# Optimization experiments

Measured on AMD Instinct MI355X. Metric: run time of the kernel, lower is better.

Reference implementation:

```python
import jax, jax.numpy as jnp
import numpy as np

N_VARS = 16
BATCH = 16
SEQ = 512
P = N_VARS * (N_VARS - 1)  # ordered pairs i != j


def setup_inputs() -> dict:
    key = jax.random.key(0)
    ks = jax.random.split(key, 12)
    n = N_VARS

    def w(k, shape, fan_in):
        return jax.random.normal(k, shape, dtype=jnp.float32) / np.sqrt(fan_in)

    z = lambda *s: jnp.zeros(s, jnp.float32)
    return {
        'data': jax.random.normal(ks[0], (BATCH, SEQ, n), dtype=jnp.float32),
        # structure learner: n*n -> 256 -> 128 -> n*n (dropout skipped / eval mode)
        'Ws1': w(ks[1], (n * n, 256), n * n), 'bs1': z(256),
        'Ws2': w(ks[2], (256, 128), 256), 'bs2': z(128),
        'Ws3': w(ks[3], (128, n * n), 128), 'bs3': z(n * n),
        # per-variable causal mechanisms (stacked): (n-1) -> 128 -> 64 -> 1
        'Wm1': w(ks[4], (n, n - 1, 128), n - 1), 'bm1': z(n, 128),
        'Wm2': w(ks[5], (n, 128, 64), 128), 'bm2': z(n, 64),
        'Wm3': w(ks[6], (n, 64), 64), 'bm3': z(n),
        # per-pair independence tests (stacked): 2 -> 32 -> 1, sigmoid
        'Wt1': w(ks[7], (P, 2, 32), 2), 'bt1': z(P, 32),
        'Wt2': w(ks[8], (P, 32), 32), 'bt2': z(P),
    }


def reference(data, Ws1, bs1, Ws2, bs2, Ws3, bs3,
              Wm1, bm1, Wm2, bm2, Wm3, bm3,
              Wt1, bt1, Wt2, bt2):
    B, S, n = data.shape
    N = B * S
    flat = data.reshape(N, n)  # [N, n] all samples

    # ---- correlations of batch-averaged series (vectorized corrcoef) ----
    avg = data.mean(axis=0)                    # [S, n]
    xc = avg - avg.mean(axis=0, keepdims=True)
    cov = xc.T @ xc                            # [n, n]
    std = jnp.sqrt(jnp.clip(jnp.diag(cov), 0.0))
    denom = std[:, None] * std[None, :]
    corr = jnp.abs(jnp.where(denom > 0, cov / jnp.where(denom > 0, denom, 1.0), 0.0))
    corr = corr * (1.0 - jnp.eye(n, dtype=corr.dtype))  # zero diagonal (i != j only)

    # ---- structure learner MLP -> sigmoid -> strict upper-tri DAG mask ----
    h = jax.nn.relu(corr.reshape(1, -1) @ Ws1 + bs1)
    h = jax.nn.relu(h @ Ws2 + bs2)
    adj = jax.nn.sigmoid(h @ Ws3 + bs3).reshape(n, n)
    adj = jnp.triu(adj, 1)

    # ---- causal mechanisms: gather-parents -> per-var MLP -> scatter ----
    idx = np.stack([[j for j in range(n) if j != v] for v in range(n)])  # [n, n-1]
    pmask = adj > 0.5
    parent_mask = pmask[idx, np.arange(n)[:, None]].astype(flat.dtype)   # [n, n-1]
    inp = flat[:, idx] * parent_mask[None]                               # [N, n, n-1]
    h1 = jax.nn.relu(jnp.einsum('nvp,vph->nvh', inp, Wm1) + bm1)         # [N, n, 128]
    h2 = jax.nn.relu(jnp.einsum('nvh,vhk->nvk', h1, Wm2) + bm2)          # [N, n, 64]
    mech = jnp.einsum('nvk,vk->nv', h2, Wm3) + bm3                       # [N, n]
    has_parents = parent_mask.sum(axis=1) > 0                            # [n]
    predictions = jnp.where(has_parents[None, :], mech, flat).reshape(B, S, n)

    # ---- batched per-pair independence tests ----
    pairs = np.array([(i, j) for i in range(n) for j in range(n) if i != j])
    pi, pj = pairs[:, 0], pairs[:, 1]
    X = jnp.stack([flat[:, pi], flat[:, pj]], axis=-1)                   # [N, P, 2]
    ht = jax.nn.relu(jnp.einsum('npc,pch->nph', X, Wt1) + bt1)           # [N, P, 32]
    s = jax.nn.sigmoid(jnp.einsum('nph,ph->np', ht, Wt2) + bt2).mean(axis=0)  # [P]
    scores = jnp.zeros((n, n), flat.dtype).at[pi, pj].set(s)

    return adj, predictions, scores
```

## Files before the change

### kernel.cpp

```cpp
#include <hip/hip_runtime.h>
#include <hip/hip_bf16.h>


typedef __attribute__((ext_vector_type(8))) short bf16x8;
typedef __attribute__((ext_vector_type(4))) short bf16x4;
typedef __attribute__((ext_vector_type(4))) float f32x4;

#define DEV __device__ __forceinline__
DEV short f2bf(float f){ __hip_bfloat16 h = __float2bfloat16(f); short s; __builtin_memcpy(&s,&h,2); return s; }

struct GraphSm {
    float avT[16 * 532];
    float part[512];
    float corr[256];
    float h1[256];
    float h2[128];
    float adj[256];
};
struct MechSm {
    short W2T[64 * 136];
    short H1[8][16 * 136];
    float W1[16 * 128];
    float B1[128];
    float B2[64];
    float W3[64];
};
struct PairSm {
    float w0[2][32], w1[2][32], bb[2][32], w2[2][32];
    float red[2][512];
    float b2s[2];
};
union SmU { GraphSm g; MechSm m; PairSm p; };

__global__ void __launch_bounds__(512, 2) k_fused(
    const float* __restrict__ data,
    const float* __restrict__ Ws1, const float* __restrict__ bs1,
    const float* __restrict__ Ws2, const float* __restrict__ bs2,
    const float* __restrict__ Ws3, const float* __restrict__ bs3,
    const float* __restrict__ Wm1, const float* __restrict__ bm1,
    const float* __restrict__ Wm2, const float* __restrict__ bm2,
    const float* __restrict__ Wm3, const float* __restrict__ bm3,
    const float* __restrict__ Wt1, const float* __restrict__ bt1,
    const float* __restrict__ Wt2, const float* __restrict__ bt2,
    float* __restrict__ out)
{
    __shared__ __align__(16) SmU sm;
    int tid = threadIdx.x, bid = blockIdx.x;

    if (bid >= 128) {
        int pb = bid - 128;
        int p0 = pb*2, p1 = p0 + 1;
        int i0 = p0 / 15, jr0 = p0 % 15;
        int j0 = jr0 + (jr0 >= i0 ? 1 : 0);
        int i1 = p1 / 15, jr1 = p1 % 15;
        int j1 = jr1 + (jr1 >= i1 ? 1 : 0);
        if (tid < 64) {
            int pp = tid >> 5, h = tid & 31;
            int p = pb*2 + pp;
            sm.p.w0[pp][h] = Wt1[p*64 + h];
            sm.p.w1[pp][h] = Wt1[p*64 + 32 + h];
            sm.p.bb[pp][h] = bt1[p*32 + h];
            sm.p.w2[pp][h] = Wt2[p*32 + h];
        }
        if (tid < 2) sm.p.b2s[tid] = bt2[pb*2 + tid];
        __syncthreads();
        float b2s0 = sm.p.b2s[0], b2s1 = sm.p.b2s[1];
        float acc0 = 0.f, acc1 = 0.f;
        float nxa0, nxb0, nxa1, nxb1;
        {
            int s = ((bid & 15) * 512) + tid;
            nxa0 = data[s*16 + i0]; nxb0 = data[s*16 + j0];
            nxa1 = data[s*16 + i1]; nxb1 = data[s*16 + j1];
        }
        for (int it = 0; it < 16; ++it) {
            float xa0 = nxa0, xb0 = nxb0, xa1 = nxa1, xb1 = nxb1;
            if (it < 15) {
                int s = (((it + 1 + bid) & 15) * 512) + tid;
                nxa0 = data[s*16 + i0]; nxb0 = data[s*16 + j0];
                nxa1 = data[s*16 + i1]; nxb1 = data[s*16 + j1];
            }
            float za0=0.f, zb0=0.f, za1=0.f, zb1=0.f;
            #pragma unroll
            for (int h = 0; h < 32; h += 2) {
                float t00 = fmaf(xa0, sm.p.w0[0][h],   fmaf(xb0, sm.p.w1[0][h],   sm.p.bb[0][h]));
                za0 = fmaf(fmaxf(t00, 0.f), sm.p.w2[0][h],   za0);
                float t01 = fmaf(xa0, sm.p.w0[0][h+1], fmaf(xb0, sm.p.w1[0][h+1], sm.p.bb[0][h+1]));
                zb0 = fmaf(fmaxf(t01, 0.f), sm.p.w2[0][h+1], zb0);
                float t10 = fmaf(xa1, sm.p.w0[1][h],   fmaf(xb1, sm.p.w1[1][h],   sm.p.bb[1][h]));
                za1 = fmaf(fmaxf(t10, 0.f), sm.p.w2[1][h],   za1);
                float t11 = fmaf(xa1, sm.p.w0[1][h+1], fmaf(xb1, sm.p.w1[1][h+1], sm.p.bb[1][h+1]));
                zb1 = fmaf(fmaxf(t11, 0.f), sm.p.w2[1][h+1], zb1);
            }
            float z0 = b2s0 + za0 + zb0;
            float z1 = b2s1 + za1 + zb1;
            acc0 += __builtin_amdgcn_rcpf(1.f + __expf(-z0));
            acc1 += __builtin_amdgcn_rcpf(1.f + __expf(-z1));
        }
        sm.p.red[0][tid] = acc0;
        sm.p.red[1][tid] = acc1;
        __syncthreads();
        for (int off = 256; off > 0; off >>= 1) {
            if (tid < off) {
                sm.p.red[0][tid] += sm.p.red[0][tid + off];
                sm.p.red[1][tid] += sm.p.red[1][tid + off];
            }
            __syncthreads();
        }
        if (tid == 0) {
            out[256 + 131072 + i0*16 + j0] = sm.p.red[0][0] * (1.f/8192.f);
            out[256 + 131072 + i1*16 + j1] = sm.p.red[1][0] * (1.f/8192.f);
        }
        return;
    }

    int v = bid >> 3, chunk = bid & 7;
    int gs0 = chunk * 1024;

    float pf_wm1[4];
    {
        #pragma unroll
        for (int r = 0; r < 4; ++r) {
            int e = tid + 512*r;
            int k = e >> 7, h = e & 127;
            pf_wm1[r] = 0.f;
            if (k != v) {
                int p = k - (k > v ? 1 : 0);
                pf_wm1[r] = Wm1[v*1920 + p*128 + h];
            }
        }
    }
    float4 pf_wm2[4];
    {
        const float* wp = Wm2 + v*8192 + tid*16;
        #pragma unroll
        for (int m4 = 0; m4 < 4; ++m4) pf_wm2[m4] = *(const float4*)&wp[m4*4];
    }
    float b1r  = bm1[v*128 + (tid & 127)];
    float b2r_ = bm2[v*64  + (tid & 63)];
    float w3r  = Wm3[v*64  + (tid & 63)];
    float bm3v = bm3[v];
    float bs1r = bs1[tid & 255];
    float bs2r = bs2[tid & 127];
    float bs3r = bs3[tid & 255];

    {
        int vb = (tid & 3) * 4;
        int sgr = ((tid >> 2) + bid*4) & 127;
        for (int k = 0; k < 4; ++k) {
            int s = sgr + k*128;
            float ax=0.f, ay=0.f, az=0.f, aw=0.f;
            #pragma unroll
            for (int b = 0; b < 16; ++b) {
                float4 d4 = *(const float4*)&data[b*8192 + s*16 + vb];
                ax += d4.x; ay += d4.y; az += d4.z; aw += d4.w;
            }
            sm.g.avT[(vb+0)*532 + s] = ax * 0.0625f;
            sm.g.avT[(vb+1)*532 + s] = ay * 0.0625f;
            sm.g.avT[(vb+2)*532 + s] = az * 0.0625f;
            sm.g.avT[(vb+3)*532 + s] = aw * 0.0625f;
        }
    }
    __syncthreads();
    if (tid < 128) {
        int vv = tid >> 3, sgm = tid & 7;
        const float* rp = &sm.g.avT[vv*532 + sgm*64];
        float a0=0.f, a1=0.f, a2=0.f, a3=0.f;
        for (int s = 0; s < 64; s += 4) {
            float4 fa = *(const float4*)&rp[s];
            a0 += fa.x; a1 += fa.y; a2 += fa.z; a3 += fa.w;
        }
        sm.g.h2[tid] = (a0+a1)+(a2+a3);
    }
    __syncthreads();
    int ci, cj; float mci, mcj;
    {
        int t = tid & 255, hh = tid >> 8;
        ci = t >> 4; cj = t & 15;
        mci = 0.f; mcj = 0.f;
        #pragma unroll
        for (int q = 0; q < 8; ++q) { mci += sm.g.h2[ci*8 + q]; mcj += sm.g.h2[cj*8 + q]; }
        mci *= (1.f/512.f); mcj *= (1.f/512.f);
        const float* pi_ = &sm.g.avT[ci*532 + hh*256];
        const float* pj_ = &sm.g.avT[cj*532 + hh*256];
        float a0=0.f, a1=0.f, a2=0.f, a3=0.f;
        #pragma unroll 8
        for (int s = 0; s < 256; s += 4) {
            float4 fa = *(const float4*)&pi_[s];
            float4 fb = *(const float4*)&pj_[s];
            a0 = fmaf(fa.x, fb.x, a0); a1 = fmaf(fa.y, fb.y, a1);
            a2 = fmaf(fa.z, fb.z, a2); a3 = fmaf(fa.w, fb.w, a3);
        }
        sm.g.part[tid] = (a0+a1)+(a2+a3);
    }
    __syncthreads();
    if (tid < 256) {
        float cij = sm.g.part[tid] + sm.g.part[256 + tid] - 512.f*mci*mcj;
        float cii = sm.g.part[ci*17] + sm.g.part[256 + ci*17] - 512.f*mci*mci;
        float cjj = sm.g.part[cj*17] + sm.g.part[256 + cj*17] - 512.f*mcj*mcj;
        float den = sqrtf(fmaxf(cii, 0.f)) * sqrtf(fmaxf(cjj, 0.f));
        sm.g.corr[tid] = (den > 0.f && ci != cj) ? fabsf(cij/den) : 0.f;
    }
    __syncthreads();

    float* red2 = sm.g.avT;

    {
        int o4 = tid & 63, ks = tid >> 6;
        int o4e = (o4 + bid*4) & 63;
        const float* W1p = Ws1 + ks*32*256 + o4e*4;
        const float* cp  = sm.g.corr + ks*32;
        float ax=0.f, ay=0.f, az=0.f, aw=0.f;
        float bx=0.f, by=0.f, bz=0.f, bw=0.f;
        #pragma unroll 8
        for (int i = 0; i < 32; i += 2) {
            float4 w0 = *(const float4*)&W1p[(i  )*256];
            float4 w1 = *(const float4*)&W1p[(i+1)*256];
            float c0 = cp[i], c1 = cp[i+1];
            ax=fmaf(c0,w0.x,ax); ay=fmaf(c0,w0.y,ay); az=fmaf(c0,w0.z,az); aw=fmaf(c0,w0.w,aw);
            bx=fmaf(c1,w1.x,bx); by=fmaf(c1,w1.y,by); bz=fmaf(c1,w1.z,bz); bw=fmaf(c1,w1.w,bw);
        }
        float4 r4; r4.x=ax+bx; r4.y=ay+by; r4.z=az+bz; r4.w=aw+bw;
        *(float4*)&red2[ks*256 + o4e*4] = r4;
    }
    __syncthreads();
    if (tid < 256) {
        float s = bs1r;
        #pragma unroll
        for (int k2 = 0; k2 < 8; ++k2) s += red2[k2*256 + tid];
        sm.g.h1[tid] = fmaxf(s, 0.f);
    }
    __syncthreads();
    {
        int o4 = tid & 31, ks = tid >> 5;
        int o4e = (o4 + bid*2) & 31;
        const float* W2p = Ws2 + ks*16*128 + o4e*4;
        const float* cp  = sm.g.h1 + ks*16;
        float ax=0.f, ay=0.f, az=0.f, aw=0.f;
        float bx=0.f, by=0.f, bz=0.f, bw=0.f;
        #pragma unroll
        for (int i = 0; i < 16; i += 2) {
            float4 w0 = *(const float4*)&W2p[(i  )*128];
            float4 w1 = *(const float4*)&W2p[(i+1)*128];
            float c0 = cp[i], c1 = cp[i+1];
            ax=fmaf(c0,w0.x,ax); ay=fmaf(c0,w0.y,ay); az=fmaf(c0,w0.z,az); aw=fmaf(c0,w0.w,aw);
            bx=fmaf(c1,w1.x,bx); by=fmaf(c1,w1.y,by); bz=fmaf(c1,w1.z,bz); bw=fmaf(c1,w1.w,bw);
        }
        float4 r4; r4.x=ax+bx; r4.y=ay+by; r4.z=az+bz; r4.w=aw+bw;
        *(float4*)&red2[ks*128 + o4e*4] = r4;
    }
    __syncthreads();
    if (tid < 128) {
        float s = bs2r;
        #pragma unroll
        for (int k2 = 0; k2 < 16; ++k2) s += red2[k2*128 + tid];
        sm.g.h2[tid] = fmaxf(s, 0.f);
    }
    __syncthreads();
    {
        int o4 = tid & 63, ks = tid >> 6;
        int o4e = (o4 + bid*4) & 63;
        const float* W3p = Ws3 + ks*16*256 + o4e*4;
        const float* cp  = sm.g.h2 + ks*16;
        float ax=0.f, ay=0.f, az=0.f, aw=0.f;
        float bx=0.f, by=0.f, bz=0.f, bw=0.f;
        #pragma unroll
        for (int i = 0; i < 16; i += 2) {
            float4 w0 = *(const float4*)&W3p[(i  )*256];
            float4 w1 = *(const float4*)&W3p[(i+1)*256];
            float c0 = cp[i], c1 = cp[i+1];
            ax=fmaf(c0,w0.x,ax); ay=fmaf(c0,w0.y,ay); az=fmaf(c0,w0.z,az); aw=fmaf(c0,w0.w,aw);
            bx=fmaf(c1,w1.x,bx); by=fmaf(c1,w1.y,by); bz=fmaf(c1,w1.z,bz); bw=fmaf(c1,w1.w,bw);
        }
        float4 r4; r4.x=ax+bx; r4.y=ay+by; r4.z=az+bz; r4.w=aw+bw;
        *(float4*)&red2[ks*256 + o4e*4] = r4;
    }
    __syncthreads();
    if (tid < 256) {
        float z = bs3r;
        #pragma unroll
        for (int k2 = 0; k2 < 8; ++k2) z += red2[k2*256 + tid];
        float a = 1.f / (1.f + expf(-z));
        int r = tid >> 4, cc = tid & 15;
        float adjv = (r < cc) ? a : 0.f;
        sm.g.adj[tid] = adjv;
        if (bid == 0) out[tid] = adjv;
    }
    if (bid == 0 && tid >= 256 && tid < 272)
        out[256 + 131072 + (tid-256)*17] = 0.f;
    __syncthreads();

    #pragma unroll
    for (int r = 0; r < 4; ++r) {
        int e = tid + 512*r;
        int k = e >> 7;
        float val = 0.f;
        if (k != v && sm.g.adj[k*16 + v] > 0.5f) val = pf_wm1[r];
        sm.m.W1[e] = val;
    }
    float hp = 0.f;
    #pragma unroll
    for (int k = 0; k < 16; ++k)
        if (k != v && sm.g.adj[k*16 + v] > 0.5f) hp = 1.f;
    #pragma unroll
    for (int m4 = 0; m4 < 4; ++m4) {
        float4 w4 = pf_wm2[m4];
        int e0 = tid*16 + m4*4;
        int h = e0 >> 6;
        int jj0 = e0 & 63;
        sm.m.W2T[(jj0+0)*136 + h] = f2bf(w4.x);
        sm.m.W2T[(jj0+1)*136 + h] = f2bf(w4.y);
        sm.m.W2T[(jj0+2)*136 + h] = f2bf(w4.z);
        sm.m.W2T[(jj0+3)*136 + h] = f2bf(w4.w);
    }
    if (tid < 128) sm.m.B1[tid] = b1r;
    else if (tid < 192) sm.m.B2[tid - 128] = b2r_;
    else if (tid < 256) sm.m.W3[tid - 192] = w3r;
    __syncthreads();

    int lane = tid & 63, wid = tid >> 6;
    int c = lane & 15, q = lane >> 4;

    bf16x8 a1f[8];
    #pragma unroll
    for (int ht = 0; ht < 8; ++ht) {
        #pragma unroll
        for (int jj = 0; jj < 8; ++jj) {
            int k = q*8 + jj;
            float w = (k < 16) ? sm.m.W1[k*128 + ht*16 + c] : 0.f;
            a1f[ht][jj] = f2bf(w);
        }
    }
    bf16x8 b2r[16];
    #pragma unroll
    for (int jt = 0; jt < 4; ++jt)
        #pragma unroll
        for (int ks = 0; ks < 4; ++ks)
            b2r[jt*4 + ks] = *(const bf16x8*)&sm.m.W2T[(jt*16 + c)*136 + ks*32 + q*8];
    float w3c[4], b2c[4];
    #pragma unroll
    for (int jt = 0; jt < 4; ++jt) { w3c[jt] = sm.m.W3[jt*16 + c]; b2c[jt] = sm.m.B2[jt*16 + c]; }

    short* h1buf = sm.m.H1[wid];
    bool act = (q < 2);

    float4 u0c, u1c;
    {
        int st0 = wid*8;
        if (act) {
            const float* xp = &data[(gs0 + st0*16 + c)*16 + q*8];
            u0c = *(const float4*)xp;
            u1c = *(const float4*)(xp + 4);
        }
    }

    for (int stl = 0; stl < 8; ++stl) {
        int st = wid*8 + stl;
        float4 u0 = u0c, u1 = u1c;
        if (stl < 7 && act) {
            const float* xp = &data[(gs0 + (st+1)*16 + c)*16 + q*8];
            u0c = *(const float4*)xp;
            u1c = *(const float4*)(xp + 4);
        }
        bf16x8 xb;
        #pragma unroll
        for (int i2 = 0; i2 < 8; ++i2) xb[i2] = 0;
        if (act) {
            xb[0] = f2bf(u0.x); xb[1] = f2bf(u0.y);
            xb[2] = f2bf(u0.z); xb[3] = f2bf(u0.w);
            xb[4] = f2bf(u1.x); xb[5] = f2bf(u1.y);
            xb[6] = f2bf(u1.z); xb[7] = f2bf(u1.w);
        }
        f32x4 c1[8];
        #pragma unroll
        for (int ht = 0; ht < 8; ++ht) c1[ht] = *(const f32x4*)&sm.m.B1[ht*16 + q*4];
        #pragma unroll
        for (int ht = 0; ht < 8; ++ht)
            c1[ht] = __builtin_amdgcn_mfma_f32_16x16x32_bf16(a1f[ht], xb, c1[ht], 0, 0, 0);
        #pragma unroll
        for (int ht = 0; ht < 8; ++ht) {
            bf16x4 pk;
            #pragma unroll
            for (int r = 0; r < 4; ++r) pk[r] = f2bf(fmaxf(c1[ht][r], 0.f));
            *(bf16x4*)&h1buf[c*136 + ht*16 + q*4] = pk;
        }
        f32x4 c2[4];
        #pragma unroll
        for (int jt = 0; jt < 4; ++jt) {
            float bi = b2c[jt];
            c2[jt] = (f32x4){bi, bi, bi, bi};
        }
        #pragma unroll
        for (int ks = 0; ks < 4; ++ks) {
            bf16x8 a2 = *(const bf16x8*)&h1buf[c*136 + ks*32 + q*8];
            #pragma unroll
            for (int jt = 0; jt < 4; ++jt)
                c2[jt] = __builtin_amdgcn_mfma_f32_16x16x32_bf16(a2, b2r[jt*4 + ks], c2[jt], 0, 0, 0);
        }
        float part[4];
        #pragma unroll
        for (int r = 0; r < 4; ++r) part[r] = 0.f;
        #pragma unroll
        for (int jt = 0; jt < 4; ++jt)
            #pragma unroll
            for (int r = 0; r < 4; ++r)
                part[r] = fmaf(fmaxf(c2[jt][r], 0.f), w3c[jt], part[r]);
        #pragma unroll
        for (int off = 1; off < 16; off <<= 1)
            #pragma unroll
            for (int r = 0; r < 4; ++r)
                part[r] += __shfl_xor(part[r], off, 16);
        if (c == 0) {
            #pragma unroll
            for (int r = 0; r < 4; ++r) {
                int s_loc = st*16 + q*4 + r;
                float mech = part[r] + bm3v;
                float xv = data[(gs0 + s_loc)*16 + v];
                out[256 + (gs0 + s_loc)*16 + v] = (hp != 0.f) ? mech : xv;
            }
        }
    }
}

extern "C" void kernel_launch(void* const* d_in, const int* in_sizes, int n_in,
                              void* d_out, int out_size, void* d_ws, size_t ws_size,
                              hipStream_t stream)
{
    const float* data = (const float*)d_in[0];
    const float* Ws1  = (const float*)d_in[1];
    const float* bs1  = (const float*)d_in[2];
    const float* Ws2  = (const float*)d_in[3];
    const float* bs2  = (const float*)d_in[4];
    const float* Ws3  = (const float*)d_in[5];
    const float* bs3  = (const float*)d_in[6];
    const float* Wm1  = (const float*)d_in[7];
    const float* bm1  = (const float*)d_in[8];
    const float* Wm2  = (const float*)d_in[9];
    const float* bm2  = (const float*)d_in[10];
    const float* Wm3  = (const float*)d_in[11];
    const float* bm3  = (const float*)d_in[12];
    const float* Wt1  = (const float*)d_in[13];
    const float* bt1  = (const float*)d_in[14];
    const float* Wt2  = (const float*)d_in[15];
    const float* bt2  = (const float*)d_in[16];
    float* out = (float*)d_out;
    (void)d_ws; (void)ws_size; (void)in_sizes; (void)n_in; (void)out_size;

    hipLaunchKernelGGL(k_fused, dim3(248), dim3(512), 0, stream,
                       data, Ws1, bs1, Ws2, bs2, Ws3, bs3,
                       Wm1, bm1, Wm2, bm2, Wm3, bm3,
                       Wt1, bt1, Wt2, bt2, out);
}
```

Baseline: 126.3 us.

## Compute graph structure once via cross-block flags instead of per-block redundancy

Result: slower. 158.8 us (+25.7%).

```diff
diff --git a/kernel.cpp b/kernel.cpp
--- a/kernel.cpp
+++ b/kernel.cpp
@@ -9,28 +9,38 @@
 #define DEV __device__ __forceinline__
 DEV short f2bf(float f){ __hip_bfloat16 h = __float2bfloat16(f); short s; __builtin_memcpy(&s,&h,2); return s; }
 
+#define WS_P1(b)   ((b)*272)
+#define WS_PM      8960
+#define WS_HP      9200
+#define WS_DUMMY   9400
+#define WS_FLAG    9600
+#define FLAG_MAGIC 0x1357F00D
+
 struct GraphSm {
-    float avT[16 * 532];
-    float part[512];
+    float sum1[256];
+    float m[16];
     float corr[256];
+    float red2[2048];
     float h1[256];
     float h2[128];
     float adj[256];
+    float pm[240];
 };
+struct ProdSm { float av[16*17]; };
 struct MechSm {
-    short W2T[64 * 136];
-    short H1[8][16 * 136];
-    float W1[16 * 128];
+    short W2T[64*136];
+    short H1[8][16*136];
+    float W1[16*128];
     float B1[128];
     float B2[64];
     float W3[64];
 };
 struct PairSm {
     float w0[2][32], w1[2][32], bb[2][32], w2[2][32];
-    float red[2][512];
+    float red0[8], red1[8];
     float b2s[2];
 };
-union SmU { GraphSm g; MechSm m; PairSm p; };
+union SmU { GraphSm g; ProdSm pr; MechSm m; PairSm p; };
 
 __global__ void __launch_bounds__(512, 2) k_fused(
     const float* __restrict__ data,
@@ -42,17 +52,19 @@
     const float* __restrict__ Wm3, const float* __restrict__ bm3,
     const float* __restrict__ Wt1, const float* __restrict__ bt1,
     const float* __restrict__ Wt2, const float* __restrict__ bt2,
-    float* __restrict__ out)
+    float* __restrict__ wsf, float* __restrict__ out)
 {
     __shared__ __align__(16) SmU sm;
+    __shared__ float pmhp[16];
     int tid = threadIdx.x, bid = blockIdx.x;
-
-    if (bid >= 128) {
-        int pb = bid - 128;
-        int p0 = pb*2, p1 = p0 + 1;
+    int* flags = (int*)(wsf + WS_FLAG);
+
+    if (bid >= 129) {
+        int pb = bid - 129;
+        int p0 = pb*2, p1p = p0 + 1;
         int i0 = p0 / 15, jr0 = p0 % 15;
         int j0 = jr0 + (jr0 >= i0 ? 1 : 0);
-        int i1 = p1 / 15, jr1 = p1 % 15;
+        int i1 = p1p / 15, jr1 = p1p % 15;
         int j1 = jr1 + (jr1 >= i1 ? 1 : 0);
         if (tid < 64) {
             int pp = tid >> 5, h = tid & 31;
@@ -66,18 +78,22 @@
         __syncthreads();
         float b2s0 = sm.p.b2s[0], b2s1 = sm.p.b2s[1];
         float acc0 = 0.f, acc1 = 0.f;
-        float nxa0, nxb0, nxa1, nxb1;
+        float a0A, b0A, a1A, b1A, a0B, b0B, a1B, b1B;
         {
-            int s = ((bid & 15) * 512) + tid;
-            nxa0 = data[s*16 + i0]; nxb0 = data[s*16 + j0];
-            nxa1 = data[s*16 + i1]; nxb1 = data[s*16 + j1];
+            int s0 = tid;
+            a0A = data[s0*16 + i0]; b0A = data[s0*16 + j0];
+            a1A = data[s0*16 + i1]; b1A = data[s0*16 + j1];
+            int s1 = 512 + tid;
+            a0B = data[s1*16 + i0]; b0B = data[s1*16 + j0];
+            a1B = data[s1*16 + i1]; b1B = data[s1*16 + j1];
         }
         for (int it = 0; it < 16; ++it) {
-            float xa0 = nxa0, xb0 = nxb0, xa1 = nxa1, xb1 = nxb1;
-            if (it < 15) {
-                int s = (((it + 1 + bid) & 15) * 512) + tid;
-                nxa0 = data[s*16 + i0]; nxb0 = data[s*16 + j0];
-                nxa1 = data[s*16 + i1]; nxb1 = data[s*16 + j1];
+            float xa0 = a0A, xb0 = b0A, xa1 = a1A, xb1 = b1A;
+            a0A = a0B; b0A = b0B; a1A = a1B; b1A = b1B;
+            if (it < 14) {
+                int s = (it + 2)*512 + tid;
+                a0B = data[s*16 + i0]; b0B = data[s*16 + j0];
+                a1B = data[s*16 + i1]; b1B = data[s*16 + j1];
             }
             float za0=0.f, zb0=0.f, za1=0.f, zb1=0.f;
             #pragma unroll
@@ -96,37 +112,211 @@
             acc0 += __builtin_amdgcn_rcpf(1.f + __expf(-z0));
             acc1 += __builtin_amdgcn_rcpf(1.f + __expf(-z1));
         }
-        sm.p.red[0][tid] = acc0;
-        sm.p.red[1][tid] = acc1;
-        __syncthreads();
-        for (int off = 256; off > 0; off >>= 1) {
-            if (tid < off) {
-                sm.p.red[0][tid] += sm.p.red[0][tid + off];
-                sm.p.red[1][tid] += sm.p.red[1][tid + off];
+        #pragma unroll
+        for (int off = 32; off > 0; off >>= 1) {
+            acc0 += __shfl_xor(acc0, off);
+            acc1 += __shfl_xor(acc1, off);
+        }
+        int lane = tid & 63, wid = tid >> 6;
+        if (lane == 0) { sm.p.red0[wid] = acc0; sm.p.red1[wid] = acc1; }
+        __syncthreads();
+        if (tid == 0) {
+            float s0 = 0.f, s1 = 0.f;
+            #pragma unroll
+            for (int w = 0; w < 8; ++w) { s0 += sm.p.red0[w]; s1 += sm.p.red1[w]; }
+            out[256 + 131072 + i0*16 + j0] = s0 * (1.f/8192.f);
+            out[256 + 131072 + i1*16 + j1] = s1 * (1.f/8192.f);
+        }
+        return;
+    }
+
+    if (bid == 0) {
+        float bs1r = bs1[tid & 255];
+        float bs2r = bs2[tid & 127];
+        float bs3r = bs3[tid & 255];
+        if (tid < 32) {
+            while (__hip_atomic_load(&flags[tid], __ATOMIC_ACQUIRE,
+                                     __HIP_MEMORY_SCOPE_AGENT) != FLAG_MAGIC)
+                __builtin_amdgcn_s_sleep(2);
+        }
+        __syncthreads();
+        __threadfence();
+        if (tid < 256) {
+            float p1 = 0.f;
+            #pragma unroll 8
+            for (int b = 0; b < 32; ++b) p1 += wsf[WS_P1(b) + tid];
+            sm.g.sum1[tid] = p1;
+        }
+        if (tid < 16) {
+            float ms = 0.f;
+            #pragma unroll 8
+            for (int b = 0; b < 32; ++b) ms += wsf[WS_P1(b) + 256 + tid];
+            sm.g.m[tid] = ms * (1.f/512.f);
+        }
+        __syncthreads();
+        if (tid < 256) {
+            int ci = tid >> 4, cj = tid & 15;
+            float mci = sm.g.m[ci], mcj = sm.g.m[cj];
+            float cij = sm.g.sum1[tid]   - 512.f*mci*mcj;
+            float cii = sm.g.sum1[ci*17] - 512.f*mci*mci;
+            float cjj = sm.g.sum1[cj*17] - 512.f*mcj*mcj;
+            float den = sqrtf(fmaxf(cii, 0.f)) * sqrtf(fmaxf(cjj, 0.f));
+            sm.g.corr[tid] = (den > 0.f && ci != cj) ? fabsf(cij/den) : 0.f;
+        }
+        __syncthreads();
+        {
+            int o4 = tid & 63, ks = tid >> 6;
+            const float* W1p = Ws1 + ks*32*256 + o4*4;
+            const float* cp  = sm.g.corr + ks*32;
+            float ax=0.f, ay=0.f, az=0.f, aw=0.f;
+            float bx=0.f, by=0.f, bz=0.f, bw=0.f;
+            #pragma unroll 8
+            for (int i = 0; i < 32; i += 2) {
+                float4 w0 = *(const float4*)&W1p[(i  )*256];
+                float4 w1 = *(const float4*)&W1p[(i+1)*256];
+                float c0 = cp[i], c1 = cp[i+1];
+                ax=fmaf(c0,w0.x,ax); ay=fmaf(c0,w0.y,ay); az=fmaf(c0,w0.z,az); aw=fmaf(c0,w0.w,aw);
+                bx=fmaf(c1,w1.x,bx); by=fmaf(c1,w1.y,by); bz=fmaf(c1,w1.z,bz); bw=fmaf(c1,w1.w,bw);
             }
-            __syncthreads();
-        }
+            float4 r4; r4.x=ax+bx; r4.y=ay+by; r4.z=az+bz; r4.w=aw+bw;
+            *(float4*)&sm.g.red2[ks*256 + o4*4] = r4;
+        }
+        __syncthreads();
+        if (tid < 256) {
+            float s = bs1r;
+            #pragma unroll
+            for (int k2 = 0; k2 < 8; ++k2) s += sm.g.red2[k2*256 + tid];
+            sm.g.h1[tid] = fmaxf(s, 0.f);
+        }
+        __syncthreads();
+        {
+            int o4 = tid & 31, ks = tid >> 5;
+            const float* W2p = Ws2 + ks*16*128 + o4*4;
+            const float* cp  = sm.g.h1 + ks*16;
+            float ax=0.f, ay=0.f, az=0.f, aw=0.f;
+            float bx=0.f, by=0.f, bz=0.f, bw=0.f;
+            #pragma unroll
+            for (int i = 0; i < 16; i += 2) {
+                float4 w0 = *(const float4*)&W2p[(i  )*128];
+                float4 w1 = *(const float4*)&W2p[(i+1)*128];
+                float c0 = cp[i], c1 = cp[i+1];
+                ax=fmaf(c0,w0.x,ax); ay=fmaf(c0,w0.y,ay); az=fmaf(c0,w0.z,az); aw=fmaf(c0,w0.w,aw);
+                bx=fmaf(c1,w1.x,bx); by=fmaf(c1,w1.y,by); bz=fmaf(c1,w1.z,bz); bw=fmaf(c1,w1.w,bw);
+            }
+            float4 r4; r4.x=ax+bx; r4.y=ay+by; r4.z=az+bz; r4.w=aw+bw;
+            *(float4*)&sm.g.red2[ks*128 + o4*4] = r4;
+        }
+        __syncthreads();
+        if (tid < 128) {
+            float s = bs2r;
+            #pragma unroll
+            for (int k2 = 0; k2 < 16; ++k2) s += sm.g.red2[k2*128 + tid];
+            sm.g.h2[tid] = fmaxf(s, 0.f);
+        }
+        __syncthreads();
+        {
+            int o4 = tid & 63, ks = tid >> 6;
+            const float* W3p = Ws3 + ks*16*256 + o4*4;
+            const float* cp  = sm.g.h2 + ks*16;
+            float ax=0.f, ay=0.f, az=0.f, aw=0.f;
+            float bx=0.f, by=0.f, bz=0.f, bw=0.f;
+            #pragma unroll
+            for (int i = 0; i < 16; i += 2) {
+                float4 w0 = *(const float4*)&W3p[(i  )*256];
+                float4 w1 = *(const float4*)&W3p[(i+1)*256];
+                float c0 = cp[i], c1 = cp[i+1];
+                ax=fmaf(c0,w0.x,ax); ay=fmaf(c0,w0.y,ay); az=fmaf(c0,w0.z,az); aw=fmaf(c0,w0.w,aw);
+                bx=fmaf(c1,w1.x,bx); by=fmaf(c1,w1.y,by); bz=fmaf(c1,w1.z,bz); bw=fmaf(c1,w1.w,bw);
+            }
+            float4 r4; r4.x=ax+bx; r4.y=ay+by; r4.z=az+bz; r4.w=aw+bw;
+            *(float4*)&sm.g.red2[ks*256 + o4*4] = r4;
+        }
+        __syncthreads();
+        if (tid < 256) {
+            float z = bs3r;
+            #pragma unroll
+            for (int k2 = 0; k2 < 8; ++k2) z += sm.g.red2[k2*256 + tid];
+            float a = 1.f / (1.f + expf(-z));
+            int r = tid >> 4, cc = tid & 15;
+            float adjv = (r < cc) ? a : 0.f;
+            sm.g.adj[tid] = adjv;
+            out[tid] = adjv;
+        }
+        if (tid >= 256 && tid < 272)
+            out[256 + 131072 + (tid-256)*17] = 0.f;
+        __syncthreads();
+        if (tid < 240) {
+            int vv = tid / 15, p = tid % 15;
+            int jj = p + (p >= vv ? 1 : 0);
+            float pmv = (sm.g.adj[jj*16 + vv] > 0.5f) ? 1.f : 0.f;
+            wsf[WS_PM + tid] = pmv;
+            sm.g.pm[tid] = pmv;
+        }
+        __syncthreads();
+        if (tid < 16) {
+            float s = 0.f;
+            #pragma unroll
+            for (int p = 0; p < 15; ++p) s += sm.g.pm[tid*15 + p];
+            wsf[WS_HP + tid] = (s > 0.f) ? 1.f : 0.f;
+        }
+        __syncthreads();
         if (tid == 0) {
-            out[256 + 131072 + i0*16 + j0] = sm.p.red[0][0] * (1.f/8192.f);
-            out[256 + 131072 + i1*16 + j1] = sm.p.red[1][0] * (1.f/8192.f);
+            __threadfence();
+            __hip_atomic_store(&flags[32], FLAG_MAGIC,
+                               __ATOMIC_RELEASE, __HIP_MEMORY_SCOPE_AGENT);
         }
         return;
     }
 
-    int v = bid >> 3, chunk = bid & 7;
+    int v = (bid - 1) >> 3, chunk = (bid - 1) & 7;
     int gs0 = chunk * 1024;
 
+    if (bid <= 32) {
+        int b = bid - 1;
+        if (tid < 256) {
+            int sl = tid >> 4, vv = tid & 15;
+            int s = b*16 + sl;
+            float acc = 0.f;
+            #pragma unroll
+            for (int bt = 0; bt < 16; ++bt) acc += data[bt*8192 + s*16 + vv];
+            sm.pr.av[sl*17 + vv] = acc * (1.f/16.f);
+        }
+        __syncthreads();
+        if (tid < 256) {
+            int i2 = tid >> 4, j2 = tid & 15;
+            float p1 = 0.f;
+            #pragma unroll
+            for (int r = 0; r < 16; ++r) p1 += sm.pr.av[r*17 + i2] * sm.pr.av[r*17 + j2];
+            wsf[WS_P1(b) + tid] = p1;
+        }
+        if (tid < 16) {
+            float ms = 0.f;
+            #pragma unroll
+            for (int r = 0; r < 16; ++r) ms += sm.pr.av[r*17 + tid];
+            wsf[WS_P1(b) + 256 + tid] = ms;
+        }
+        __syncthreads();
+        if (tid == 0) {
+            __threadfence();
+            __hip_atomic_store(&flags[b], FLAG_MAGIC,
+                               __ATOMIC_RELEASE, __HIP_MEMORY_SCOPE_AGENT);
+        }
+        unsigned xr = 0;
+        { uint4 u = ((const uint4*)Ws1)[b*512 + tid]; xr ^= u.x^u.y^u.z^u.w; }
+        if (tid < 256) { uint4 u = ((const uint4*)Ws2)[b*256 + tid];       xr ^= u.x^u.y^u.z^u.w; }
+        else           { uint4 u = ((const uint4*)Ws3)[b*256 + tid - 256]; xr ^= u.x^u.y^u.z^u.w; }
+        if (xr == 0x9E3779B9u) wsf[WS_DUMMY] = 0.f;
+    }
+
     float pf_wm1[4];
-    {
-        #pragma unroll
-        for (int r = 0; r < 4; ++r) {
-            int e = tid + 512*r;
-            int k = e >> 7, h = e & 127;
-            pf_wm1[r] = 0.f;
-            if (k != v) {
-                int p = k - (k > v ? 1 : 0);
-                pf_wm1[r] = Wm1[v*1920 + p*128 + h];
-            }
+    #pragma unroll
+    for (int r = 0; r < 4; ++r) {
+        int e = tid + 512*r;
+        int k = e >> 7, h = e & 127;
+        pf_wm1[r] = 0.f;
+        if (k != v) {
+            int p = k - (k > v ? 1 : 0);
+            pf_wm1[r] = Wm1[v*1920 + p*128 + h];
         }
     }
     float4 pf_wm2[4];
@@ -136,171 +326,10 @@
         for (int m4 = 0; m4 < 4; ++m4) pf_wm2[m4] = *(const float4*)&wp[m4*4];
     }
     float b1r  = bm1[v*128 + (tid & 127)];
-    float b2r_ = bm2[v*64  + (tid & 63)];
+    float b2rv = bm2[v*64  + (tid & 63)];
     float w3r  = Wm3[v*64  + (tid & 63)];
     float bm3v = bm3[v];
-    float bs1r = bs1[tid & 255];
-    float bs2r = bs2[tid & 127];
-    float bs3r = bs3[tid & 255];
-
-    {
-        int vb = (tid & 3) * 4;
-        int sgr = ((tid >> 2) + bid*4) & 127;
-        for (int k = 0; k < 4; ++k) {
-            int s = sgr + k*128;
-            float ax=0.f, ay=0.f, az=0.f, aw=0.f;
-            #pragma unroll
-            for (int b = 0; b < 16; ++b) {
-                float4 d4 = *(const float4*)&data[b*8192 + s*16 + vb];
-                ax += d4.x; ay += d4.y; az += d4.z; aw += d4.w;
-            }
-            sm.g.avT[(vb+0)*532 + s] = ax * 0.0625f;
-            sm.g.avT[(vb+1)*532 + s] = ay * 0.0625f;
-            sm.g.avT[(vb+2)*532 + s] = az * 0.0625f;
-            sm.g.avT[(vb+3)*532 + s] = aw * 0.0625f;
-        }
-    }
-    __syncthreads();
-    if (tid < 128) {
-        int vv = tid >> 3, sgm = tid & 7;
-        const float* rp = &sm.g.avT[vv*532 + sgm*64];
-        float a0=0.f, a1=0.f, a2=0.f, a3=0.f;
-        for (int s = 0; s < 64; s += 4) {
-            float4 fa = *(const float4*)&rp[s];
-            a0 += fa.x; a1 += fa.y; a2 += fa.z; a3 += fa.w;
-        }
-        sm.g.h2[tid] = (a0+a1)+(a2+a3);
-    }
-    __syncthreads();
-    int ci, cj; float mci, mcj;
-    {
-        int t = tid & 255, hh = tid >> 8;
-        ci = t >> 4; cj = t & 15;
-        mci = 0.f; mcj = 0.f;
-        #pragma unroll
-        for (int q = 0; q < 8; ++q) { mci += sm.g.h2[ci*8 + q]; mcj += sm.g.h2[cj*8 + q]; }
-        mci *= (1.f/512.f); mcj *= (1.f/512.f);
-        const float* pi_ = &sm.g.avT[ci*532 + hh*256];
-        const float* pj_ = &sm.g.avT[cj*532 + hh*256];
-        float a0=0.f, a1=0.f, a2=0.f, a3=0.f;
-        #pragma unroll 8
-        for (int s = 0; s < 256; s += 4) {
-            float4 fa = *(const float4*)&pi_[s];
-            float4 fb = *(const float4*)&pj_[s];
-            a0 = fmaf(fa.x, fb.x, a0); a1 = fmaf(fa.y, fb.y, a1);
-            a2 = fmaf(fa.z, fb.z, a2); a3 = fmaf(fa.w, fb.w, a3);
-        }
-        sm.g.part[tid] = (a0+a1)+(a2+a3);
-    }
-    __syncthreads();
-    if (tid < 256) {
-        float cij = sm.g.part[tid] + sm.g.part[256 + tid] - 512.f*mci*mcj;
-        float cii = sm.g.part[ci*17] + sm.g.part[256 + ci*17] - 512.f*mci*mci;
-        float cjj = sm.g.part[cj*17] + sm.g.part[256 + cj*17] - 512.f*mcj*mcj;
-        float den = sqrtf(fmaxf(cii, 0.f)) * sqrtf(fmaxf(cjj, 0.f));
-        sm.g.corr[tid] = (den > 0.f && ci != cj) ? fabsf(cij/den) : 0.f;
-    }
-    __syncthreads();
-
-    float* red2 = sm.g.avT;
-
-    {
-        int o4 = tid & 63, ks = tid >> 6;
-        int o4e = (o4 + bid*4) & 63;
-        const float* W1p = Ws1 + ks*32*256 + o4e*4;
-        const float* cp  = sm.g.corr + ks*32;
-        float ax=0.f, ay=0.f, az=0.f, aw=0.f;
-        float bx=0.f, by=0.f, bz=0.f, bw=0.f;
-        #pragma unroll 8
-        for (int i = 0; i < 32; i += 2) {
-            float4 w0 = *(const float4*)&W1p[(i  )*256];
-            float4 w1 = *(const float4*)&W1p[(i+1)*256];
-            float c0 = cp[i], c1 = cp[i+1];
-            ax=fmaf(c0,w0.x,ax); ay=fmaf(c0,w0.y,ay); az=fmaf(c0,w0.z,az); aw=fmaf(c0,w0.w,aw);
-            bx=fmaf(c1,w1.x,bx); by=fmaf(c1,w1.y,by); bz=fmaf(c1,w1.z,bz); bw=fmaf(c1,w1.w,bw);
-        }
-        float4 r4; r4.x=ax+bx; r4.y=ay+by; r4.z=az+bz; r4.w=aw+bw;
-        *(float4*)&red2[ks*256 + o4e*4] = r4;
-    }
-    __syncthreads();
-    if (tid < 256) {
-        float s = bs1r;
-        #pragma unroll
-        for (int k2 = 0; k2 < 8; ++k2) s += red2[k2*256 + tid];
-        sm.g.h1[tid] = fmaxf(s, 0.f);
-    }
-    __syncthreads();
-    {
-        int o4 = tid & 31, ks = tid >> 5;
-        int o4e = (o4 + bid*2) & 31;
-        const float* W2p = Ws2 + ks*16*128 + o4e*4;
-        const float* cp  = sm.g.h1 + ks*16;
-        float ax=0.f, ay=0.f, az=0.f, aw=0.f;
-        float bx=0.f, by=0.f, bz=0.f, bw=0.f;
-        #pragma unroll
-        for (int i = 0; i < 16; i += 2) {
-            float4 w0 = *(const float4*)&W2p[(i  )*128];
-            float4 w1 = *(const float4*)&W2p[(i+1)*128];
-            float c0 = cp[i], c1 = cp[i+1];
-            ax=fmaf(c0,w0.x,ax); ay=fmaf(c0,w0.y,ay); az=fmaf(c0,w0.z,az); aw=fmaf(c0,w0.w,aw);
-            bx=fmaf(c1,w1.x,bx); by=fmaf(c1,w1.y,by); bz=fmaf(c1,w1.z,bz); bw=fmaf(c1,w1.w,bw);
-        }
-        float4 r4; r4.x=ax+bx; r4.y=ay+by; r4.z=az+bz; r4.w=aw+bw;
-        *(float4*)&red2[ks*128 + o4e*4] = r4;
-    }
-    __syncthreads();
-    if (tid < 128) {
-        float s = bs2r;
-        #pragma unroll
-        for (int k2 = 0; k2 < 16; ++k2) s += red2[k2*128 + tid];
-        sm.g.h2[tid] = fmaxf(s, 0.f);
-    }
-    __syncthreads();
-    {
-        int o4 = tid & 63, ks = tid >> 6;
-        int o4e = (o4 + bid*4) & 63;
-        const float* W3p = Ws3 + ks*16*256 + o4e*4;
-        const float* cp  = sm.g.h2 + ks*16;
-        float ax=0.f, ay=0.f, az=0.f, aw=0.f;
-        float bx=0.f, by=0.f, bz=0.f, bw=0.f;
-        #pragma unroll
-        for (int i = 0; i < 16; i += 2) {
-            float4 w0 = *(const float4*)&W3p[(i  )*256];
-            float4 w1 = *(const float4*)&W3p[(i+1)*256];
-            float c0 = cp[i], c1 = cp[i+1];
-            ax=fmaf(c0,w0.x,ax); ay=fmaf(c0,w0.y,ay); az=fmaf(c0,w0.z,az); aw=fmaf(c0,w0.w,aw);
-            bx=fmaf(c1,w1.x,bx); by=fmaf(c1,w1.y,by); bz=fmaf(c1,w1.z,bz); bw=fmaf(c1,w1.w,bw);
-        }
-        float4 r4; r4.x=ax+bx; r4.y=ay+by; r4.z=az+bz; r4.w=aw+bw;
-        *(float4*)&red2[ks*256 + o4e*4] = r4;
-    }
-    __syncthreads();
-    if (tid < 256) {
-        float z = bs3r;
-        #pragma unroll
-        for (int k2 = 0; k2 < 8; ++k2) z += red2[k2*256 + tid];
-        float a = 1.f / (1.f + expf(-z));
-        int r = tid >> 4, cc = tid & 15;
-        float adjv = (r < cc) ? a : 0.f;
-        sm.g.adj[tid] = adjv;
-        if (bid == 0) out[tid] = adjv;
-    }
-    if (bid == 0 && tid >= 256 && tid < 272)
-        out[256 + 131072 + (tid-256)*17] = 0.f;
-    __syncthreads();
-
-    #pragma unroll
-    for (int r = 0; r < 4; ++r) {
-        int e = tid + 512*r;
-        int k = e >> 7;
-        float val = 0.f;
-        if (k != v && sm.g.adj[k*16 + v] > 0.5f) val = pf_wm1[r];
-        sm.m.W1[e] = val;
-    }
-    float hp = 0.f;
-    #pragma unroll
-    for (int k = 0; k < 16; ++k)
-        if (k != v && sm.g.adj[k*16 + v] > 0.5f) hp = 1.f;
+
     #pragma unroll
     for (int m4 = 0; m4 < 4; ++m4) {
         float4 w4 = pf_wm2[m4];
@@ -313,23 +342,12 @@
         sm.m.W2T[(jj0+3)*136 + h] = f2bf(w4.w);
     }
     if (tid < 128) sm.m.B1[tid] = b1r;
-    else if (tid < 192) sm.m.B2[tid - 128] = b2r_;
+    else if (tid < 192) sm.m.B2[tid - 128] = b2rv;
     else if (tid < 256) sm.m.W3[tid - 192] = w3r;
     __syncthreads();
 
     int lane = tid & 63, wid = tid >> 6;
     int c = lane & 15, q = lane >> 4;
-
-    bf16x8 a1f[8];
-    #pragma unroll
-    for (int ht = 0; ht < 8; ++ht) {
-        #pragma unroll
-        for (int jj = 0; jj < 8; ++jj) {
-            int k = q*8 + jj;
-            float w = (k < 16) ? sm.m.W1[k*128 + ht*16 + c] : 0.f;
-            a1f[ht][jj] = f2bf(w);
-        }
-    }
     bf16x8 b2r[16];
     #pragma unroll
     for (int jt = 0; jt < 4; ++jt)
@@ -339,17 +357,48 @@
     float w3c[4], b2c[4];
     #pragma unroll
     for (int jt = 0; jt < 4; ++jt) { w3c[jt] = sm.m.W3[jt*16 + c]; b2c[jt] = sm.m.B2[jt*16 + c]; }
-
     short* h1buf = sm.m.H1[wid];
     bool act = (q < 2);
-
     float4 u0c, u1c;
-    {
-        int st0 = wid*8;
-        if (act) {
-            const float* xp = &data[(gs0 + st0*16 + c)*16 + q*8];
-            u0c = *(const float4*)xp;
-            u1c = *(const float4*)(xp + 4);
+    if (act) {
+        const float* xp = &data[(gs0 + wid*8*16 + c)*16 + q*8];
+        u0c = *(const float4*)xp;
+        u1c = *(const float4*)(xp + 4);
+    }
+
+    if (tid == 0) {
+        while (__hip_atomic_load(&flags[32], __ATOMIC_RELAXED,
+                                 __HIP_MEMORY_SCOPE_AGENT) != FLAG_MAGIC)
+            __builtin_amdgcn_s_sleep(2);
+    }
+    __syncthreads();
+    __threadfence();
+    if (tid < 16) pmhp[tid] = (tid < 15) ? wsf[WS_PM + v*15 + tid]
+                                         : wsf[WS_HP + v];
+    __syncthreads();
+
+    #pragma unroll
+    for (int r = 0; r < 4; ++r) {
+        int e = tid + 512*r;
+        int k = e >> 7;
+        float val = 0.f;
+        if (k != v) {
+            int p = k - (k > v ? 1 : 0);
+            val = pf_wm1[r] * pmhp[p];
+        }
+        sm.m.W1[e] = val;
+    }
+    float hp = pmhp[15];
+    __syncthreads();
+
+    bf16x8 a1f[8];
+    #pragma unroll
+    for (int ht = 0; ht < 8; ++ht) {
+        #pragma unroll
+        for (int jj = 0; jj < 8; ++jj) {
+            int k = q*8 + jj;
+            float w = (k < 16) ? sm.m.W1[k*128 + ht*16 + c] : 0.f;
+            a1f[ht][jj] = f2bf(w);
         }
     }
 
@@ -442,11 +491,12 @@
     const float* bt1  = (const float*)d_in[14];
     const float* Wt2  = (const float*)d_in[15];
     const float* bt2  = (const float*)d_in[16];
+    float* wsf = (float*)d_ws;
     float* out = (float*)d_out;
-    (void)d_ws; (void)ws_size; (void)in_sizes; (void)n_in; (void)out_size;
-
-    hipLaunchKernelGGL(k_fused, dim3(248), dim3(512), 0, stream,
+    (void)in_sizes; (void)n_in; (void)out_size; (void)ws_size;
+
+    hipLaunchKernelGGL(k_fused, dim3(249), dim3(512), 0, stream,
                        data, Ws1, bs1, Ws2, bs2, Ws3, bs3,
                        Wm1, bm1, Wm2, bm2, Wm3, bm3,
-                       Wt1, bt1, Wt2, bt2, out);
+                       Wt1, bt1, Wt2, bt2, wsf, out);
 }
```
